# Performance work log

Hardware: AMD Instinct MI355X
Metric: run time of the kernel (lower is better)

Reference implementation:

```python
import jax, jax.numpy as jnp
import numpy as np

N = 100000   # nodes
G = 256      # graphs
E = 120000   # edges per relation
IN = 162
HID = 128
R = 5
L = 2        # extra RGCN layers beyond the initial one


def setup_inputs() -> dict:
    key = jax.random.key(0)
    ks = jax.random.split(key, 24)
    s = 0.05
    inp = {
        "X": jax.random.normal(ks[0], (N, IN), jnp.float32),
        "batch": jnp.sort(jax.random.randint(ks[6], (N,), 0, G)),
    }
    for i in range(R):
        inp[f"edge_index{i+1}"] = jax.random.randint(ks[1 + i], (2, E), 0, N)
    # RGCN initial layer params
    inp["W0"] = jax.random.normal(ks[7], (R, IN, HID), jnp.float32) * s
    inp["root0"] = jax.random.normal(ks[8], (IN, HID), jnp.float32) * s
    inp["b0"] = jnp.zeros((HID,), jnp.float32)
    # stacked params for the L hidden RGCN layers
    inp["Wl"] = jax.random.normal(ks[9], (L, R, HID, HID), jnp.float32) * s
    inp["rootl"] = jax.random.normal(ks[10], (L, HID, HID), jnp.float32) * s
    inp["bl"] = jnp.zeros((L, HID), jnp.float32)
    # classification head
    inp["Wc1"] = jax.random.normal(ks[11], (HID, HID), jnp.float32) * s
    inp["bc1"] = jnp.zeros((HID,), jnp.float32)
    inp["Wc2"] = jax.random.normal(ks[12], (HID, HID), jnp.float32) * s
    inp["bc2"] = jnp.zeros((HID,), jnp.float32)
    inp["Wc3"] = jax.random.normal(ks[13], (HID, 1), jnp.float32) * s
    inp["bc3"] = jnp.zeros((1,), jnp.float32)
    return inp


def _seg_mean(msg, dst, num):
    # scatter-mean over destination nodes (PyG RGCNConv uses aggr='mean' per relation)
    s = jax.ops.segment_sum(msg, dst, num_segments=num)
    c = jax.ops.segment_sum(jnp.ones(msg.shape[0], msg.dtype), dst, num_segments=num)
    return s / jnp.maximum(c, 1.0)[:, None]


def _rgcn(x, W, root, b, src, dst):
    # src, dst: [R, E]; W: [R, d_in, d_out]
    msgs = jnp.einsum("ref,rfh->reh", x[src], W)          # [R, E, HID]
    agg = jax.vmap(_seg_mean, in_axes=(0, 0, None))(msgs, dst, N)  # [R, N, HID]
    return x @ root + b + agg.sum(0)


def reference(X, edge_index1, edge_index2, edge_index3, edge_index4, edge_index5,
              batch, W0, root0, b0, Wl, rootl, bl, Wc1, bc1, Wc2, bc2, Wc3, bc3):
    ei = jnp.stack([edge_index1, edge_index2, edge_index3, edge_index4, edge_index5])  # [R,2,E]
    src, dst = ei[:, 0, :], ei[:, 1, :]
    h = jax.nn.relu(_rgcn(X, W0, root0, b0, src, dst))
    for l in range(L):
        h = jax.nn.relu(_rgcn(h, Wl[l], rootl[l], bl[l], src, dst))
    # mean readout over graphs
    s = jax.ops.segment_sum(h, batch, num_segments=G)
    c = jax.ops.segment_sum(jnp.ones((N,), h.dtype), batch, num_segments=G)
    read = s / jnp.maximum(c, 1.0)[:, None]
    h = jax.nn.relu(read @ Wc1 + bc1)
    h = jax.nn.relu(h @ Wc2 + bc2)
    return h @ Wc3 + bc3
```

## Files before the change

### kernel.cpp

```cpp
#include <hip/hip_runtime.h>

#define N_NODES 100000
#define NPAD    100096
#define NTILES  782
#define G_GRAPHS 256
#define IN_F 162
#define KPAD0 192
#define HID 128
#define R_REL 5
#define L_LAYERS 2
#define M5 (R_REL * N_NODES)

typedef __attribute__((ext_vector_type(8))) short bf16x8;
typedef __attribute__((ext_vector_type(4))) float f32x4;

__device__ __forceinline__ short f2bf(float f) {
    union { float f; unsigned u; } v; v.f = f;
    unsigned r = (v.u + 0x7fffu + ((v.u >> 16) & 1u)) >> 16;
    return (short)r;
}
__device__ __forceinline__ float bf2f(unsigned short u) {
    union { unsigned u; float f; } v; v.u = ((unsigned)u) << 16;
    return v.f;
}

__global__ void k_count(const int* e0, const int* e1, const int* e2,
                        const int* e3, const int* e4, int* cnt, int E) {
    int gid = blockIdx.x * 256 + threadIdx.x;
    if (gid >= R_REL * E) return;
    int r = gid / E, e = gid - r * E;
    const int* ei = (r == 0) ? e0 : (r == 1) ? e1 : (r == 2) ? e2 : (r == 3) ? e3 : e4;
    atomicAdd(&cnt[r * N_NODES + ei[E + e]], 1);
}

__global__ __launch_bounds__(256) void k_scan1(const int* __restrict__ cnt,
                                               int* __restrict__ off, int* __restrict__ bsum) {
    __shared__ int ts[256];
    int t = threadIdx.x;
    int base = blockIdx.x * 1024 + t * 4;
    int v[4];
    #pragma unroll
    for (int j = 0; j < 4; j++) {
        int d = base + j;
        int s = 0;
        if (d < N_NODES) {
            #pragma unroll
            for (int r = 0; r < R_REL; r++) s += cnt[r * N_NODES + d];
        }
        v[j] = s;
    }
    int tsum = v[0] + v[1] + v[2] + v[3];
    ts[t] = tsum; __syncthreads();
    for (int o = 1; o < 256; o <<= 1) {
        int x = (t >= o) ? ts[t - o] : 0;
        __syncthreads();
        ts[t] += x;
        __syncthreads();
    }
    if (t == 255) bsum[blockIdx.x] = ts[255];
    int run = ts[t] - tsum;
    #pragma unroll
    for (int j = 0; j < 4; j++) { if (base + j < N_NODES) off[base + j] = run; run += v[j]; }
}

__global__ __launch_bounds__(512) void k_scan2(int* bsum, int nblk) {
    __shared__ int ts[512];
    int t = threadIdx.x;
    int v = (t < nblk) ? bsum[t] : 0;
    ts[t] = v; __syncthreads();
    for (int o = 1; o < 512; o <<= 1) {
        int x = (t >= o) ? ts[t - o] : 0;
        __syncthreads();
        ts[t] += x;
        __syncthreads();
    }
    if (t < nblk) bsum[t] = ts[t] - v;
}

__global__ void k_scan3(const int* __restrict__ off, const int* __restrict__ bsum,
                        int* __restrict__ mstart, int* __restrict__ mcur,
                        const int* __restrict__ cnt, float* __restrict__ invc) {
    int i = blockIdx.x * 256 + threadIdx.x;
    if (i >= N_NODES) return;
    int o = off[i] + bsum[i >> 10];
    mstart[i] = o;
    mcur[i] = o;
    int tc = 0;
    #pragma unroll
    for (int r = 0; r < R_REL; r++) {
        int c = cnt[r * N_NODES + i];
        tc += c;
        invc[r * N_NODES + i] = 1.0f / (float)max(c, 1);
    }
    if (i == N_NODES - 1) mstart[N_NODES] = o + tc;
}

__global__ void k_fill(const int* e0, const int* e1, const int* e2,
                       const int* e3, const int* e4, int* mcur,
                       const float* __restrict__ invc,
                       int* __restrict__ mrec, float* __restrict__ mw, int E) {
    int gid = blockIdx.x * 256 + threadIdx.x;
    if (gid >= R_REL * E) return;
    int r = gid / E, e = gid - r * E;
    const int* ei = (r == 0) ? e0 : (r == 1) ? e1 : (r == 2) ? e2 : (r == 3) ? e3 : e4;
    int src = ei[e], dst = ei[E + e];
    int pos = atomicAdd(&mcur[dst], 1);
    mrec[pos] = ((1 + r) * NPAD + src) * HID;
    mw[pos] = invc[r * N_NODES + dst];
}

__global__ void k_tw0(const float* __restrict__ root0, const float* __restrict__ W0,
                      short* __restrict__ out) {
    int gid = blockIdx.x * 256 + threadIdx.x;
    if (gid >= 6 * 128 * KPAD0) return;
    int chunk = gid / (128 * KPAD0);
    int rem = gid - chunk * 128 * KPAD0;
    int col = rem / KPAD0;
    int k = rem - col * KPAD0;
    float v = 0.f;
    if (k < IN_F)
        v = (chunk == 0) ? root0[k * HID + col]
                         : W0[((size_t)(chunk - 1) * IN_F + k) * HID + col];
    out[gid] = f2bf(v);
}

__global__ void k_twl(const float* __restrict__ rootl, const float* __restrict__ Wl,
                      short* __restrict__ out) {
    int gid = blockIdx.x * 256 + threadIdx.x;
    if (gid >= L_LAYERS * 6 * 128 * HID) return;
    int l = gid / (6 * 128 * HID);
    int rem = gid - l * 6 * 128 * HID;
    int chunk = rem / (128 * HID);
    int rem2 = rem - chunk * 128 * HID;
    int col = rem2 / HID;
    int k = rem2 - col * HID;
    float v = (chunk == 0) ? rootl[((size_t)l * HID + k) * HID + col]
                           : Wl[(((size_t)l * R_REL + (chunk - 1)) * HID + k) * HID + col];
    out[gid] = f2bf(v);
}

template<int SEG, bool A_F32, int MINW>
__global__ __launch_bounds__(256, MINW)
void gemm_reg(const void* __restrict__ Av, const short* __restrict__ Wt,
              unsigned short* __restrict__ Y) {
    constexpr int KSEG = SEG / 32;
    constexpr int SBP = SEG + 8;
    __shared__ short Bs[128 * SBP];
    const int tid = threadIdx.x;
    const int row0 = blockIdx.x * 128;
    const int lane = tid & 63, wv = tid >> 6;
    const int quad = lane >> 4, l16 = lane & 15;
    const int wr0 = (wv >> 1) * 64, wc0 = (wv & 1) * 64;

    bf16x8 af[KSEG][4];
    #pragma unroll
    for (int i = 0; i < 4; i++) {
        int grow = row0 + wr0 + i * 16 + l16;
        if (A_F32) {
            const float* rp = (const float*)Av + (size_t)grow * IN_F;
            bool ok = grow < N_NODES;
            #pragma unroll
            for (int kb = 0; kb < KSEG; kb++) {
                bf16x8 v;
                if (kb < 5) {
                    int k = kb * 32 + quad * 8;
                    #pragma unroll
                    for (int h = 0; h < 4; h++) {
                        float2 f2 = ok ? *(const float2*)(rp + k + 2 * h)
                                       : make_float2(0.f, 0.f);
                        v[2 * h] = f2bf(f2.x); v[2 * h + 1] = f2bf(f2.y);
                    }
                } else {
                    int k = 160 + quad * 8;
                    #pragma unroll
                    for (int j = 0; j < 8; j++) {
                        int kk = k + j;
                        float f = (ok && kk < IN_F) ? rp[kk] : 0.f;
                        v[j] = f2bf(f);
                    }
                }
                af[kb][i] = v;
            }
        } else {
            const unsigned short* Ab = (const unsigned short*)Av;
            #pragma unroll
            for (int kb = 0; kb < KSEG; kb++)
                af[kb][i] = *(const bf16x8*)&Ab[(size_t)grow * SEG + kb * 32 + quad * 8];
        }
    }

    for (int chunk = 0; chunk < 6; chunk++) {
        if (chunk) __syncthreads();
        const short* Wc = Wt + (size_t)chunk * 128 * SEG;
        for (int c = tid; c < 128 * (SEG / 8); c += 256) {
            int r = c / (SEG / 8), c8 = (c - r * (SEG / 8)) * 8;
            *(bf16x8*)&Bs[r * SBP + c8] = *(const bf16x8*)&Wc[r * SEG + c8];
        }
        __syncthreads();

        f32x4 acc[4][4];
        #pragma unroll
        for (int i = 0; i < 4; i++)
            #pragma unroll
            for (int j = 0; j < 4; j++) acc[i][j] = (f32x4){0.f, 0.f, 0.f, 0.f};

        #pragma unroll
        for (int kb = 0; kb < KSEG; kb++) {
            bf16x8 bfr[4];
            #pragma unroll
            for (int j = 0; j < 4; j++)
                bfr[j] = *(const bf16x8*)&Bs[(wc0 + j * 16 + l16) * SBP + kb * 32 + quad * 8];
            #pragma unroll
            for (int i = 0; i < 4; i++)
                #pragma unroll
                for (int j = 0; j < 4; j++)
                    acc[i][j] = __builtin_amdgcn_mfma_f32_16x16x32_bf16(af[kb][i], bfr[j], acc[i][j], 0, 0, 0);
        }
        __syncthreads();

        #pragma unroll
        for (int i = 0; i < 4; i++)
            #pragma unroll
            for (int j = 0; j < 4; j++)
                #pragma unroll
                for (int reg = 0; reg < 4; reg++)
                    Bs[(wr0 + i * 16 + quad * 4 + reg) * SBP + wc0 + j * 16 + l16] =
                        f2bf(acc[i][j][reg]);
        __syncthreads();

        unsigned short* Yc = Y + (size_t)chunk * NPAD * HID + (size_t)row0 * HID;
        #pragma unroll
        for (int s = 0; s < 8; s++) {
            int row = (tid >> 4) + s * 16;
            int col = (tid & 15) * 8;
            bf16x8 v = *(const bf16x8*)&Bs[row * SBP + col];
            *(bf16x8*)&Yc[(size_t)row * HID + col] = v;
        }
    }
}

__global__ __launch_bounds__(256)
void aggregate(const unsigned short* __restrict__ Yall, const int* __restrict__ mstart,
               const int* __restrict__ mrec, const float* __restrict__ mw,
               const float* __restrict__ bias, unsigned short* __restrict__ hout) {
    int wid = (blockIdx.x * 256 + threadIdx.x) >> 6;
    int lane = threadIdx.x & 63;
    if (wid >= N_NODES) return;
    int d = wid;
    int s = mstart[d], e = mstart[d + 1];

    float2 b2 = *(const float2*)&bias[lane * 2];
    unsigned rv = *(const unsigned*)&Yall[(size_t)d * HID + lane * 2];
    float s0 = b2.x + bf2f((unsigned short)(rv & 0xffff));
    float s1 = b2.y + bf2f((unsigned short)(rv >> 16));

    for (int base = s; base < e; base += 64) {
        int m = min(e - base, 64);
        int rec = 0; float w = 0.f;
        if (lane < m) { rec = mrec[base + lane]; w = mw[base + lane]; }
        for (int j = 0; j < m; j += 8) {
            int g = min(8, m - j);
            unsigned v[8]; float wj[8];
            #pragma unroll
            for (int t = 0; t < 8; t++) {
                if (t < g) {
                    int off = __shfl(rec, j + t, 64);
                    wj[t] = __shfl(w, j + t, 64);
                    v[t] = *(const unsigned*)&Yall[(size_t)off + lane * 2];
                } else { v[t] = 0u; wj[t] = 0.f; }
            }
            #pragma unroll
            for (int t = 0; t < 8; t++) {
                s0 += wj[t] * bf2f((unsigned short)(v[t] & 0xffff));
                s1 += wj[t] * bf2f((unsigned short)(v[t] >> 16));
            }
        }
    }
    unsigned lo = (unsigned short)f2bf(fmaxf(s0, 0.f));
    unsigned hi = (unsigned short)f2bf(fmaxf(s1, 0.f));
    *(unsigned*)&hout[(size_t)d * HID + lane * 2] = lo | (hi << 16);
}

__global__ __launch_bounds__(128)
void k_pool(const unsigned short* __restrict__ h, const int* __restrict__ batch,
            float* __restrict__ pooled) {
    int c = threadIdx.x;
    int start = blockIdx.x * 128;
    if (start >= N_NODES) return;
    int end = min(start + 128, N_NODES);
    int g = batch[start];
    float s = 0.f;
    for (int i = start; i < end; i++) {
        int gi = batch[i];
        if (gi != g) { atomicAdd(&pooled[g * HID + c], s); s = 0.f; g = gi; }
        s += bf2f(h[(size_t)i * HID + c]);
    }
    atomicAdd(&pooled[g * HID + c], s);
}

__device__ int lower_bound_i(const int* a, int n, int v) {
    int lo = 0, hi = n;
    while (lo < hi) {
        int mid = (lo + hi) >> 1;
        if (a[mid] < v) lo = mid + 1; else hi = mid;
    }
    return lo;
}

__global__ __launch_bounds__(128)
void k_mlp(const float* __restrict__ pooled, const int* __restrict__ batch,
           const float* __restrict__ Wc1, const float* __restrict__ bc1,
           const float* __restrict__ Wc2, const float* __restrict__ bc2,
           const float* __restrict__ Wc3, const float* __restrict__ bc3,
           float* __restrict__ out) {
    int g = blockIdx.x;
    int c = threadIdx.x;
    __shared__ int range[2];
    if (c == 0) range[0] = lower_bound_i(batch, N_NODES, g);
    if (c == 1) range[1] = lower_bound_i(batch, N_NODES, g + 1);
    __syncthreads();
    float denom = fmaxf((float)(range[1] - range[0]), 1.0f);
    __shared__ float row[HID], h1[HID], h2[HID];
    row[c] = pooled[g * HID + c] / denom;
    __syncthreads();
    float acc = bc1[c];
    for (int k = 0; k < HID; k++) acc += row[k] * Wc1[k * HID + c];
    h1[c] = fmaxf(acc, 0.f);
    __syncthreads();
    acc = bc2[c];
    for (int k = 0; k < HID; k++) acc += h1[k] * Wc2[k * HID + c];
    h2[c] = fmaxf(acc, 0.f);
    __syncthreads();
    float t = h2[c] * Wc3[c];
    for (int off = 32; off > 0; off >>= 1) t += __shfl_down(t, off, 64);
    __shared__ float part[2];
    if ((c & 63) == 0) part[c >> 6] = t;
    __syncthreads();
    if (c == 0) out[g] = part[0] + part[1] + bc3[0];
}

extern "C" void kernel_launch(void* const* d_in, const int* in_sizes, int n_in,
                              void* d_out, int out_size, void* d_ws, size_t ws_size,
                              hipStream_t stream) {
    const float* X     = (const float*)d_in[0];
    const int*   batch = (const int*)d_in[1];
    const int*   e0 = (const int*)d_in[2];
    const int*   e1 = (const int*)d_in[3];
    const int*   e2 = (const int*)d_in[4];
    const int*   e3 = (const int*)d_in[5];
    const int*   e4 = (const int*)d_in[6];
    const float* W0    = (const float*)d_in[7];
    const float* root0 = (const float*)d_in[8];
    const float* b0    = (const float*)d_in[9];
    const float* Wl    = (const float*)d_in[10];
    const float* rootl = (const float*)d_in[11];
    const float* bl    = (const float*)d_in[12];
    const float* Wc1   = (const float*)d_in[13];
    const float* bc1   = (const float*)d_in[14];
    const float* Wc2   = (const float*)d_in[15];
    const float* bc2   = (const float*)d_in[16];
    const float* Wc3   = (const float*)d_in[17];
    const float* bc3   = (const float*)d_in[18];
    const int E = in_sizes[2] / 2;
    const int NE = R_REL * E;

    char* base = (char*)d_ws;
    size_t o = 0;
    auto carve = [&](size_t bytes) -> char* {
        char* p = base + o;
        o = (o + bytes + 255) & ~(size_t)255;
        return p;
    };
    unsigned short* Y    = (unsigned short*)carve((size_t)6 * NPAD * HID * 2);
    unsigned short* hA   = (unsigned short*)carve((size_t)NPAD * HID * 2);
    unsigned short* hB   = (unsigned short*)carve((size_t)NPAD * HID * 2);
    int*   cnt    = (int*)carve((size_t)M5 * 4);
    float* invc   = (float*)carve((size_t)M5 * 4);
    int*   offsc  = (int*)carve((size_t)N_NODES * 4);
    int*   mstart = (int*)carve((size_t)(N_NODES + 1) * 4);
    int*   mcur   = (int*)carve((size_t)N_NODES * 4);
    int*   mrec   = (int*)carve((size_t)NE * 4);
    float* mw     = (float*)carve((size_t)NE * 4);
    int*   bsum   = (int*)carve(2048);
    float* pooled = (float*)carve((size_t)G_GRAPHS * HID * 4);
    short* Wt0    = (short*)carve((size_t)6 * 128 * KPAD0 * 2);
    short* Wtl    = (short*)carve((size_t)L_LAYERS * 6 * 128 * HID * 2);

    hipMemsetAsync(cnt, 0, (size_t)M5 * 4, stream);
    hipMemsetAsync(pooled, 0, (size_t)G_GRAPHS * HID * 4, stream);
    int eg = (NE + 255) / 256;
    k_count<<<eg, 256, 0, stream>>>(e0, e1, e2, e3, e4, cnt, E);
    int nblk = (N_NODES + 1023) / 1024;
    k_scan1<<<nblk, 256, 0, stream>>>(cnt, offsc, bsum);
    k_scan2<<<1, 512, 0, stream>>>(bsum, nblk);
    k_scan3<<<(N_NODES + 255) / 256, 256, 0, stream>>>(offsc, bsum, mstart, mcur, cnt, invc);
    k_fill<<<eg, 256, 0, stream>>>(e0, e1, e2, e3, e4, mcur, invc, mrec, mw, E);
    k_tw0<<<(6 * 128 * KPAD0 + 255) / 256, 256, 0, stream>>>(root0, W0, Wt0);
    k_twl<<<(L_LAYERS * 6 * 128 * HID + 255) / 256, 256, 0, stream>>>(rootl, Wl, Wtl);

    int agg_grid = (N_NODES + 3) / 4;

    gemm_reg<KPAD0, true, 2><<<NTILES, 256, 0, stream>>>(X, Wt0, Y);
    aggregate<<<agg_grid, 256, 0, stream>>>(Y, mstart, mrec, mw, b0, hA);

    unsigned short* hin = hA; unsigned short* hout = hB;
    for (int l = 0; l < L_LAYERS; l++) {
        gemm_reg<HID, false, 3><<<NTILES, 256, 0, stream>>>(hin, Wtl + (size_t)l * 6 * 128 * HID, Y);
        aggregate<<<agg_grid, 256, 0, stream>>>(Y, mstart, mrec, mw, bl + (size_t)l * HID, hout);
        unsigned short* t = hin; hin = hout; hout = t;
    }

    k_pool<<<(N_NODES + 127) / 128, 128, 0, stream>>>(hin, batch, pooled);
    k_mlp<<<G_GRAPHS, 128, 0, stream>>>(pooled, batch, Wc1, bc1, Wc2, bc2, Wc3, bc3, (float*)d_out);
}
```

Before: 738.7 us.

## Split GEMM across weight chunks per block with XCD-aware tile mapping and A prefetch

The GEMM previously looped over all 6 weight chunks per 128-row tile, keeping the whole A tile in registers. Now each block handles one (row tile, chunk) pair, giving 6x more blocks. Block IDs are remapped so that the six chunks of a row tile land on the same XCD and share its L2. A-fragments are loaded from global memory with a register double-buffer across K steps. The trade-off is that each A tile is re-read six times from memory/L2 in exchange for more parallelism and lower register pressure.

```diff
diff --git a/kernel.cpp b/kernel.cpp
--- a/kernel.cpp
+++ b/kernel.cpp
@@ -139,103 +139,123 @@
     out[gid] = f2bf(v);
 }
 
-template<int SEG, bool A_F32, int MINW>
-__global__ __launch_bounds__(256, MINW)
-void gemm_reg(const void* __restrict__ Av, const short* __restrict__ Wt,
-              unsigned short* __restrict__ Y) {
+template<int SEG, bool A_F32>
+__device__ __forceinline__ bf16x8 load_af(const void* __restrict__ Av, int grow,
+                                          int kb, int quad) {
+    bf16x8 v = (bf16x8){0, 0, 0, 0, 0, 0, 0, 0};
+    if (A_F32) {
+        if (grow < N_NODES) {
+            const float* rp = (const float*)Av + (size_t)grow * IN_F;
+            int k = kb * 32 + quad * 8;
+            if (k + 8 <= IN_F) {
+                #pragma unroll
+                for (int h = 0; h < 4; h++) {
+                    float2 f2 = *(const float2*)(rp + k + 2 * h);
+                    v[2 * h] = f2bf(f2.x); v[2 * h + 1] = f2bf(f2.y);
+                }
+            } else {
+                #pragma unroll
+                for (int j = 0; j < 8; j++) {
+                    int kk = k + j;
+                    float f = (kk < IN_F) ? rp[kk] : 0.f;
+                    v[j] = f2bf(f);
+                }
+            }
+        }
+    } else {
+        v = *(const bf16x8*)((const unsigned short*)Av + (size_t)grow * SEG + kb * 32 + quad * 8);
+    }
+    return v;
+}
+
+template<int SEG, bool A_F32>
+__global__ __launch_bounds__(256)
+void gemm_direct(const void* __restrict__ Av, const short* __restrict__ Wt,
+                 unsigned short* __restrict__ Y) {
     constexpr int KSEG = SEG / 32;
+    constexpr int PF = (KSEG > 4) ? 2 : KSEG;
     constexpr int SBP = SEG + 8;
     __shared__ short Bs[128 * SBP];
+
+    int bid = blockIdx.x;
+    int xcd = bid & 7, slot = bid >> 3;
+    int tl = slot / 6, chunk = slot - tl * 6;
+    int rt = tl * 8 + xcd;
+    if (rt >= NTILES) return;
+    const int row0 = rt * 128;
+
     const int tid = threadIdx.x;
-    const int row0 = blockIdx.x * 128;
     const int lane = tid & 63, wv = tid >> 6;
     const int quad = lane >> 4, l16 = lane & 15;
     const int wr0 = (wv >> 1) * 64, wc0 = (wv & 1) * 64;
 
-    bf16x8 af[KSEG][4];
-    #pragma unroll
-    for (int i = 0; i < 4; i++) {
-        int grow = row0 + wr0 + i * 16 + l16;
-        if (A_F32) {
-            const float* rp = (const float*)Av + (size_t)grow * IN_F;
-            bool ok = grow < N_NODES;
-            #pragma unroll
-            for (int kb = 0; kb < KSEG; kb++) {
-                bf16x8 v;
-                if (kb < 5) {
-                    int k = kb * 32 + quad * 8;
-                    #pragma unroll
-                    for (int h = 0; h < 4; h++) {
-                        float2 f2 = ok ? *(const float2*)(rp + k + 2 * h)
-                                       : make_float2(0.f, 0.f);
-                        v[2 * h] = f2bf(f2.x); v[2 * h + 1] = f2bf(f2.y);
-                    }
-                } else {
-                    int k = 160 + quad * 8;
-                    #pragma unroll
-                    for (int j = 0; j < 8; j++) {
-                        int kk = k + j;
-                        float f = (ok && kk < IN_F) ? rp[kk] : 0.f;
-                        v[j] = f2bf(f);
-                    }
-                }
-                af[kb][i] = v;
-            }
-        } else {
-            const unsigned short* Ab = (const unsigned short*)Av;
-            #pragma unroll
-            for (int kb = 0; kb < KSEG; kb++)
-                af[kb][i] = *(const bf16x8*)&Ab[(size_t)grow * SEG + kb * 32 + quad * 8];
-        }
-    }
-
-    for (int chunk = 0; chunk < 6; chunk++) {
-        if (chunk) __syncthreads();
-        const short* Wc = Wt + (size_t)chunk * 128 * SEG;
-        for (int c = tid; c < 128 * (SEG / 8); c += 256) {
-            int r = c / (SEG / 8), c8 = (c - r * (SEG / 8)) * 8;
-            *(bf16x8*)&Bs[r * SBP + c8] = *(const bf16x8*)&Wc[r * SEG + c8];
-        }
-        __syncthreads();
-
-        f32x4 acc[4][4];
+    bf16x8 cur[PF][4], nxt[PF][4];
+    #pragma unroll
+    for (int p = 0; p < PF; p++)
         #pragma unroll
         for (int i = 0; i < 4; i++)
-            #pragma unroll
-            for (int j = 0; j < 4; j++) acc[i][j] = (f32x4){0.f, 0.f, 0.f, 0.f};
-
+            cur[p][i] = load_af<SEG, A_F32>(Av, row0 + wr0 + i * 16 + l16, p, quad);
+
+    const short* Wc = Wt + (size_t)chunk * 128 * SEG;
+    for (int c = tid; c < 128 * (SEG / 8); c += 256) {
+        int r = c / (SEG / 8), c8 = (c - r * (SEG / 8)) * 8;
+        *(bf16x8*)&Bs[r * SBP + c8] = *(const bf16x8*)&Wc[r * SEG + c8];
+    }
+    __syncthreads();
+
+    f32x4 acc[4][4];
+    #pragma unroll
+    for (int i = 0; i < 4; i++)
         #pragma unroll
-        for (int kb = 0; kb < KSEG; kb++) {
+        for (int j = 0; j < 4; j++) acc[i][j] = (f32x4){0.f, 0.f, 0.f, 0.f};
+
+    for (int kb = 0; kb < KSEG; kb += PF) {
+        if (kb + PF < KSEG) {
+            #pragma unroll
+            for (int p = 0; p < PF; p++)
+                #pragma unroll
+                for (int i = 0; i < 4; i++)
+                    nxt[p][i] = load_af<SEG, A_F32>(Av, row0 + wr0 + i * 16 + l16,
+                                                    kb + PF + p, quad);
+        }
+        #pragma unroll
+        for (int p = 0; p < PF; p++) {
+            int k0 = (kb + p) * 32;
             bf16x8 bfr[4];
             #pragma unroll
             for (int j = 0; j < 4; j++)
-                bfr[j] = *(const bf16x8*)&Bs[(wc0 + j * 16 + l16) * SBP + kb * 32 + quad * 8];
+                bfr[j] = *(const bf16x8*)&Bs[(wc0 + j * 16 + l16) * SBP + k0 + quad * 8];
             #pragma unroll
             for (int i = 0; i < 4; i++)
                 #pragma unroll
                 for (int j = 0; j < 4; j++)
-                    acc[i][j] = __builtin_amdgcn_mfma_f32_16x16x32_bf16(af[kb][i], bfr[j], acc[i][j], 0, 0, 0);
+                    acc[i][j] = __builtin_amdgcn_mfma_f32_16x16x32_bf16(cur[p][i], bfr[j], acc[i][j], 0, 0, 0);
         }
-        __syncthreads();
-
         #pragma unroll
-        for (int i = 0; i < 4; i++)
-            #pragma unroll
-            for (int j = 0; j < 4; j++)
-                #pragma unroll
-                for (int reg = 0; reg < 4; reg++)
-                    Bs[(wr0 + i * 16 + quad * 4 + reg) * SBP + wc0 + j * 16 + l16] =
-                        f2bf(acc[i][j][reg]);
-        __syncthreads();
-
-        unsigned short* Yc = Y + (size_t)chunk * NPAD * HID + (size_t)row0 * HID;
+        for (int p = 0; p < PF; p++)
+            #pragma unroll
+            for (int i = 0; i < 4; i++)
+                cur[p][i] = nxt[p][i];
+    }
+    __syncthreads();
+
+    #pragma unroll
+    for (int i = 0; i < 4; i++)
         #pragma unroll
-        for (int s = 0; s < 8; s++) {
-            int row = (tid >> 4) + s * 16;
-            int col = (tid & 15) * 8;
-            bf16x8 v = *(const bf16x8*)&Bs[row * SBP + col];
-            *(bf16x8*)&Yc[(size_t)row * HID + col] = v;
-        }
+        for (int j = 0; j < 4; j++)
+            #pragma unroll
+            for (int reg = 0; reg < 4; reg++)
+                Bs[(wr0 + i * 16 + quad * 4 + reg) * SBP + wc0 + j * 16 + l16] =
+                    f2bf(acc[i][j][reg]);
+    __syncthreads();
+
+    unsigned short* Yc = Y + (size_t)chunk * NPAD * HID + (size_t)row0 * HID;
+    #pragma unroll
+    for (int s = 0; s < 8; s++) {
+        int row = (tid >> 4) + s * 16;
+        int col = (tid & 15) * 8;
+        bf16x8 v = *(const bf16x8*)&Bs[row * SBP + col];
+        *(bf16x8*)&Yc[(size_t)row * HID + col] = v;
     }
 }
 
@@ -398,14 +418,15 @@
     k_tw0<<<(6 * 128 * KPAD0 + 255) / 256, 256, 0, stream>>>(root0, W0, Wt0);
     k_twl<<<(L_LAYERS * 6 * 128 * HID + 255) / 256, 256, 0, stream>>>(rootl, Wl, Wtl);
 
+    int ggrid = 8 * 98 * 6;
     int agg_grid = (N_NODES + 3) / 4;
 
-    gemm_reg<KPAD0, true, 2><<<NTILES, 256, 0, stream>>>(X, Wt0, Y);
+    gemm_direct<KPAD0, true><<<ggrid, 256, 0, stream>>>(X, Wt0, Y);
     aggregate<<<agg_grid, 256, 0, stream>>>(Y, mstart, mrec, mw, b0, hA);
 
     unsigned short* hin = hA; unsigned short* hout = hB;
     for (int l = 0; l < L_LAYERS; l++) {
-        gemm_reg<HID, false, 3><<<NTILES, 256, 0, stream>>>(hin, Wtl + (size_t)l * 6 * 128 * HID, Y);
+        gemm_direct<HID, false><<<ggrid, 256, 0, stream>>>(hin, Wtl + (size_t)l * 6 * 128 * HID, Y);
         aggregate<<<agg_grid, 256, 0, stream>>>(Y, mstart, mrec, mw, bl + (size_t)l * HID, hout);
         unsigned short* t = hin; hin = hout; hout = t;
     }
```

New measurement: 727.4 us. Within noise of the previous version (-1.5%).
